# Kernel optimization log

Measured on AMD Instinct MI355X. Metric: run time of the kernel, lower is better.

The kernel has to match this reference:

```python
import jax, jax.numpy as jnp
import numpy as np

N = 100000      # total sampled nodes
NT = 20000      # target (destination) nodes
E = 2000000     # edges
IN = 128        # in_dim
OUT = 64        # out_channels (heads=1, concat)
NEG_SLOPE = 0.2 # GATConv default negative_slope


def setup_inputs() -> dict:
    key = jax.random.key(0)
    ks = jax.random.split(key, 6)
    x = jax.random.normal(ks[0], (N, IN), dtype=jnp.float32)
    edge_src = jax.random.randint(ks[1], (E,), 0, N)
    edge_dst = jax.random.randint(ks[2], (E,), 0, NT)
    # GATConv params: shared lin for src/dst (in_channels is int), att vectors, bias
    W = jax.random.normal(ks[3], (IN, OUT), dtype=jnp.float32) / np.sqrt(IN).astype(np.float32)
    att_src = jax.random.normal(ks[4], (OUT,), dtype=jnp.float32)
    att_dst = jax.random.normal(ks[5], (OUT,), dtype=jnp.float32)
    bias = jnp.zeros((OUT,), dtype=jnp.float32)
    return {"x": x, "edge_src": edge_src, "edge_dst": edge_dst,
            "W": W, "att_src": att_src, "att_dst": att_dst, "bias": bias,
            "num_target": NT}


def reference(x, edge_src, edge_dst, W, att_src, att_dst, bias, num_target):
    # Linear transform (lin_src == lin_dst in PyG GATConv when in_channels is int)
    x_proj = x @ W                      # [N, OUT]
    x_dst = x_proj[:num_target]         # [NT, OUT] target nodes are x[:num_target]
    # Per-node attention logits
    a_src = x_proj @ att_src            # [N]
    a_dst = x_dst @ att_dst             # [NT]
    # Edge logits + LeakyReLU
    e = jax.nn.leaky_relu(a_src[edge_src] + a_dst[edge_dst], NEG_SLOPE)  # [E]
    # Segment softmax over edges grouped by destination
    m = jax.ops.segment_max(e, edge_dst, num_segments=num_target)
    m = jnp.where(jnp.isneginf(m), jnp.float32(0.0), m)  # empty segments
    p = jnp.exp(e - m[edge_dst])
    denom = jax.ops.segment_sum(p, edge_dst, num_segments=num_target)
    alpha = p / (denom[edge_dst] + jnp.float32(1e-16))   # PyG softmax eps
    # Weighted scatter-aggregate of source features
    out = jax.ops.segment_sum(alpha[:, None] * x_proj[edge_src], edge_dst,
                              num_segments=num_target)   # [NT, OUT]
    return out + bias
```

## Files before the change

kernel.cpp:

```cpp
#include <hip/hip_runtime.h>

#define IN_DIM 128
#define OUT_DIM 64
#define NEG_SLOPE 0.2f

#define NBUCK 625
#define BCAP 4096
#define CHUNK 8192

typedef __attribute__((ext_vector_type(8))) short short8v;
typedef __attribute__((ext_vector_type(4))) float f32x4;

__device__ __forceinline__ unsigned pack_bf16(float a, float b) {
    unsigned ua = __float_as_uint(a), ub = __float_as_uint(b);
    ua += 0x7FFFu + ((ua >> 16) & 1u);
    ub += 0x7FFFu + ((ub >> 16) & 1u);
    return (ua >> 16) | (ub & 0xFFFF0000u);
}

__device__ __forceinline__ short8v mk8(unsigned a, unsigned b, unsigned c, unsigned d) {
    union { uint4 u; short8v s; } z;
    z.u = make_uint4(a, b, c, d);
    return z.s;
}

__device__ __forceinline__ int slice_of(unsigned src, float inv_sdiv) {
    int s = (int)((float)src * inv_sdiv);
    return s > 3 ? 3 : s;
}

__global__ __launch_bounds__(256) void prep_kernel(
    const float* __restrict__ W, unsigned* __restrict__ w_hi,
    unsigned* __restrict__ w_lo, int* __restrict__ bcursor)
{
    if (blockIdx.x == 4) {
        for (int i = threadIdx.x; i < NBUCK; i += 256) bcursor[i] = 0;
        return;
    }
    int g = blockIdx.x * 256 + threadIdx.x;
    int kb = g >> 6, col = g & 63;
    unsigned uh[4], ul[4];
#pragma unroll
    for (int i = 0; i < 4; ++i) {
        float a = W[(kb * 8 + 2 * i) * 64 + col];
        float b = W[(kb * 8 + 2 * i + 1) * 64 + col];
        unsigned h = pack_bf16(a, b);
        float la = a - __uint_as_float(h << 16);
        float lb = b - __uint_as_float(h & 0xFFFF0000u);
        uh[i] = h;
        ul[i] = pack_bf16(la, lb);
    }
    *(uint4*)(w_hi + g * 4) = make_uint4(uh[0], uh[1], uh[2], uh[3]);
    *(uint4*)(w_lo + g * 4) = make_uint4(ul[0], ul[1], ul[2], ul[3]);
}

__global__ __launch_bounds__(1024) void fused_kernel(
    const float* __restrict__ x,
    const unsigned* __restrict__ w_hi, const unsigned* __restrict__ w_lo,
    const float* __restrict__ att_src, const float* __restrict__ att_dst,
    const int* __restrict__ edge_src, const int* __restrict__ edge_dst,
    int* __restrict__ bcursor, unsigned* __restrict__ inter,
    unsigned* __restrict__ x_bf, float* __restrict__ a_src,
    float* __restrict__ a_dst, int N, int NT, int E, int nchunk)
{
    __shared__ __align__(16) union SMem {
        struct {
            unsigned stage[CHUNK];
            int hist[NBUCK];
            int loff[NBUCK];
            int gbase[NBUCK];
            int cur[NBUCK];
            int wsum[16];
        } p;
        float C[128 * 64];
    } U;

    const int t = threadIdx.x;

    if ((int)blockIdx.x < nchunk) {
        const int c0 = blockIdx.x * CHUNK;
        const int cnt = min(CHUNK, E - c0);

        for (int i = t; i < NBUCK; i += 1024) U.p.hist[i] = 0;
        __syncthreads();

        unsigned pk[8];
        int nmine = 0;
        const int i0 = 8 * t;
        if (i0 + 8 <= cnt) {
            int4 s0 = *(const int4*)(edge_src + c0 + i0);
            int4 s1 = *(const int4*)(edge_src + c0 + i0 + 4);
            int4 d0 = *(const int4*)(edge_dst + c0 + i0);
            int4 d1 = *(const int4*)(edge_dst + c0 + i0 + 4);
            pk[0] = ((unsigned)d0.x << 17) | (unsigned)s0.x;
            pk[1] = ((unsigned)d0.y << 17) | (unsigned)s0.y;
            pk[2] = ((unsigned)d0.z << 17) | (unsigned)s0.z;
            pk[3] = ((unsigned)d0.w << 17) | (unsigned)s0.w;
            pk[4] = ((unsigned)d1.x << 17) | (unsigned)s1.x;
            pk[5] = ((unsigned)d1.y << 17) | (unsigned)s1.y;
            pk[6] = ((unsigned)d1.z << 17) | (unsigned)s1.z;
            pk[7] = ((unsigned)d1.w << 17) | (unsigned)s1.w;
            nmine = 8;
        } else {
#pragma unroll
            for (int k = 0; k < 8; ++k) {
                int i = i0 + k;
                if (i < cnt) {
                    pk[k] = ((unsigned)edge_dst[c0 + i] << 17) | (unsigned)edge_src[c0 + i];
                    nmine = k + 1;
                }
            }
        }
#pragma unroll
        for (int k = 0; k < 8; ++k)
            if (k < nmine) atomicAdd(&U.p.hist[pk[k] >> 22], 1);
        __syncthreads();

        {
            const int lane = t & 63, w = t >> 6;
            int v = (t < NBUCK) ? U.p.hist[t] : 0;
            int scan = v;
#pragma unroll
            for (int off = 1; off < 64; off <<= 1) {
                int o = __shfl_up(scan, off);
                if (lane >= off) scan += o;
            }
            if (lane == 63) U.p.wsum[w] = scan;
            __syncthreads();
            int wpre = 0;
#pragma unroll
            for (int i = 0; i < 16; ++i)
                if (i < w) wpre += U.p.wsum[i];
            int excl = wpre + scan - v;
            if (t < NBUCK) {
                U.p.loff[t] = excl;
                U.p.cur[t]  = excl;
                if (v > 0) U.p.gbase[t] = t * BCAP + atomicAdd(&bcursor[t], v);
            }
        }
        __syncthreads();

#pragma unroll
        for (int k = 0; k < 8; ++k)
            if (k < nmine) {
                unsigned v = pk[k];
                int p = atomicAdd(&U.p.cur[v >> 22], 1);
                U.p.stage[p] = v;
            }
        __syncthreads();

        for (int i = t; i < cnt; i += 1024) {
            unsigned v = U.p.stage[i];
            int b = v >> 22;
            int pos = U.p.gbase[b] + (i - U.p.loff[b]);
            if (pos < (b + 1) * BCAP) inter[pos] = v;
        }
        return;
    }

    const int bid = blockIdx.x - nchunk;
    const int sub = t >> 8;
    const int t2  = t & 255;
    const int lane = t2 & 63;
    const int w    = t2 >> 6;
    const int r0   = bid * 512 + sub * 128;
    const int rsub = lane & 15;
    const int kg   = lane >> 4;

    const int r1 = min(r0 + 32 * w + rsub,      N - 1);
    const int r2 = min(r0 + 32 * w + 16 + rsub, N - 1);
    const float* xrow1 = x + (size_t)r1 * IN_DIM + kg * 8;
    const float* xrow2 = x + (size_t)r2 * IN_DIM + kg * 8;

    float4 xv[16];
#pragma unroll
    for (int j = 0; j < 8; ++j)
        xv[j] = *(const float4*)(xrow1 + (j >> 1) * 32 + (j & 1) * 4);
#pragma unroll
    for (int j = 0; j < 8; ++j)
        xv[8 + j] = *(const float4*)(xrow2 + (j >> 1) * 32 + (j & 1) * 4);
    __builtin_amdgcn_sched_barrier(0);

    short8v ah[2][4], al[2][4];
#pragma unroll
    for (int rf = 0; rf < 2; ++rf)
#pragma unroll
        for (int ks = 0; ks < 4; ++ks) {
            float4 v0 = xv[8 * rf + 2 * ks], v1 = xv[8 * rf + 2 * ks + 1];
            unsigned h0 = pack_bf16(v0.x, v0.y);
            unsigned h1 = pack_bf16(v0.z, v0.w);
            unsigned h2 = pack_bf16(v1.x, v1.y);
            unsigned h3 = pack_bf16(v1.z, v1.w);
            unsigned l0 = pack_bf16(v0.x - __uint_as_float(h0 << 16),
                                    v0.y - __uint_as_float(h0 & 0xFFFF0000u));
            unsigned l1 = pack_bf16(v0.z - __uint_as_float(h1 << 16),
                                    v0.w - __uint_as_float(h1 & 0xFFFF0000u));
            unsigned l2 = pack_bf16(v1.x - __uint_as_float(h2 << 16),
                                    v1.y - __uint_as_float(h2 & 0xFFFF0000u));
            unsigned l3 = pack_bf16(v1.z - __uint_as_float(h3 << 16),
                                    v1.w - __uint_as_float(h3 & 0xFFFF0000u));
            ah[rf][ks] = mk8(h0, h1, h2, h3);
            al[rf][ks] = mk8(l0, l1, l2, l3);
        }

    f32x4 acc[2][4];
#pragma unroll
    for (int rf = 0; rf < 2; ++rf)
#pragma unroll
        for (int cf = 0; cf < 4; ++cf) acc[rf][cf] = f32x4{0.f, 0.f, 0.f, 0.f};

#pragma unroll
    for (int ks = 0; ks < 4; ++ks) {
        const int kb = 4 * ks + kg;
        const unsigned* bhp = w_hi + (kb * 64 + rsub) * 4;
        const unsigned* blp = w_lo + (kb * 64 + rsub) * 4;
        short8v bh[4], bl[4];
#pragma unroll
        for (int cf = 0; cf < 4; ++cf) {
            bh[cf] = *(const short8v*)(bhp + cf * 64);
            bl[cf] = *(const short8v*)(blp + cf * 64);
        }
#pragma unroll
        for (int cf = 0; cf < 4; ++cf) {
#pragma unroll
            for (int rf = 0; rf < 2; ++rf) {
                acc[rf][cf] = __builtin_amdgcn_mfma_f32_16x16x32_bf16(ah[rf][ks], bh[cf], acc[rf][cf], 0, 0, 0);
                acc[rf][cf] = __builtin_amdgcn_mfma_f32_16x16x32_bf16(al[rf][ks], bh[cf], acc[rf][cf], 0, 0, 0);
                acc[rf][cf] = __builtin_amdgcn_mfma_f32_16x16x32_bf16(ah[rf][ks], bl[cf], acc[rf][cf], 0, 0, 0);
            }
        }
    }

    for (int ph = 0; ph < 4; ++ph) {
        if (sub == ph) {
#pragma unroll
            for (int rf = 0; rf < 2; ++rf)
#pragma unroll
                for (int cf = 0; cf < 4; ++cf)
#pragma unroll
                    for (int j = 0; j < 4; ++j) {
                        int row = 32 * w + 16 * rf + 4 * kg + j;
                        int col = 16 * cf + rsub;
                        U.C[row * 64 + ((col + 4 * row) & 63)] = acc[rf][cf][j];
                    }
        }
        __syncthreads();
        if (sub == ph) {
            const int row = t2 >> 1;
            const int h   = t2 & 1;
            const int rr  = r0 + row;
            float v[32];
#pragma unroll
            for (int j = 0; j < 8; ++j) {
                int s = (32 * h + 4 * j + 4 * row) & 63;
                float4 f = *(const float4*)(U.C + row * 64 + s);
                v[4 * j + 0] = f.x; v[4 * j + 1] = f.y;
                v[4 * j + 2] = f.z; v[4 * j + 3] = f.w;
            }
            if (rr < N) {
                unsigned pk[16];
#pragma unroll
                for (int m = 0; m < 16; ++m)
                    pk[m] = pack_bf16(v[2 * m], v[2 * m + 1]);
                unsigned* dst = x_bf + (size_t)rr * 32 + h * 16;
                *(uint4*)(dst + 0)  = make_uint4(pk[0], pk[1], pk[2], pk[3]);
                *(uint4*)(dst + 4)  = make_uint4(pk[4], pk[5], pk[6], pk[7]);
                *(uint4*)(dst + 8)  = make_uint4(pk[8], pk[9], pk[10], pk[11]);
                *(uint4*)(dst + 12) = make_uint4(pk[12], pk[13], pk[14], pk[15]);

                float ps = 0.f, pd = 0.f;
#pragma unroll
                for (int i = 0; i < 32; ++i) {
                    ps = fmaf(v[i], att_src[32 * h + i], ps);
                    pd = fmaf(v[i], att_dst[32 * h + i], pd);
                }
                ps += __shfl_xor(ps, 1);
                pd += __shfl_xor(pd, 1);
                if (h == 0) {
                    a_src[rr] = ps;
                    if (rr < NT) a_dst[rr] = pd;
                }
            }
        }
        __syncthreads();
    }
}

#define LRELU_EXP(a) __expf(((a) > 0.f ? (a) : NEG_SLOPE * (a)))

__global__ __launch_bounds__(512) void agg_kernel(
    const int* __restrict__ bcursor, const unsigned* __restrict__ inter,
    const float* __restrict__ a_src, const float* __restrict__ a_dst,
    const unsigned* __restrict__ x_bf, const float* __restrict__ bias,
    float* __restrict__ out, int NT, float inv_sdiv)
{
    __shared__ unsigned ssrc[BCAP];
    __shared__ int cnt[128], off_[128], cur[128];

    const int b = blockIdx.x;
    const int t = threadIdx.x;
    const int base = b * BCAP;
    const int n = min(bcursor[b], BCAP);

    for (int i = t; i < 128; i += 512) cnt[i] = 0;
    __syncthreads();

    unsigned ev[8];
    int kk[8];
#pragma unroll
    for (int k = 0; k < 8; ++k) {
        int i = t + 512 * k;
        ev[k] = 0xFFFFFFFFu;
        kk[k] = 0;
        if (i < n) {
            unsigned v = inter[base + i];
            ev[k] = v;
            kk[k] = (slice_of(v & 0x1FFFFu, inv_sdiv) << 5) | ((v >> 17) & 31);
            atomicAdd(&cnt[kk[k]], 1);
        }
    }
    __syncthreads();

    if (t == 0) {
        int r = 0;
#pragma unroll
        for (int j = 0; j < 128; ++j) { off_[j] = r; r += cnt[j]; }
    }
    __syncthreads();
    if (t < 128) cur[t] = off_[t];
    __syncthreads();

#pragma unroll
    for (int k = 0; k < 8; ++k)
        if (ev[k] != 0xFFFFFFFFu) {
            int p = atomicAdd(&cur[kk[k]], 1);
            ssrc[p] = ev[k] & 0x1FFFFu;
        }
    __syncthreads();

    const int lane = t & 63;
    const int w    = t >> 6;
    const int q    = lane >> 4;
    const int g    = (lane >> 3) & 1;
    const int sub  = lane & 7;

    const int ld  = 4 * w + q;
    const int tgt = b * 32 + ld;
    const float ad = (tgt < NT) ? a_dst[tgt] : 0.f;

    float dl = 0.f;
    float acc[8];
#pragma unroll
    for (int k = 0; k < 8; ++k) acc[k] = 0.f;

    for (int s = 0; s < 4; ++s) {
        const int key = (s << 5) | ld;
        const int lo = off_[key];
        const int nn = cnt[key];

        int ncmax = (nn + 15) >> 4;
        ncmax = max(ncmax, __shfl_xor(ncmax, 16));
        ncmax = max(ncmax, __shfl_xor(ncmax, 32));

        for (int c = 0; c < ncmax; ++c) {
            const int el = 16 * c + 8 * g + sub;
            const bool valid = el < nn;
            const int sA = valid ? (int)ssrc[lo + el] : 0;

            int s8[8];
#pragma unroll
            for (int j = 0; j < 8; ++j) s8[j] = __shfl(sA, 16 * q + 8 * g + j);

            uint4 v[8];
#pragma unroll
            for (int j = 0; j < 8; ++j)
                v[j] = *(const uint4*)(x_bf + (size_t)s8[j] * 32 + sub * 4);

            const float aA = a_src[sA];
            const float pA = valid ? LRELU_EXP(aA + ad) : 0.f;
            dl += pA;

            float p8[8];
#pragma unroll
            for (int j = 0; j < 8; ++j) p8[j] = __shfl(pA, 16 * q + 8 * g + j);

#pragma unroll
            for (int j = 0; j < 8; ++j) {
                const float p = p8[j];
                acc[0] = fmaf(p, __uint_as_float(v[j].x << 16), acc[0]);
                acc[1] = fmaf(p, __uint_as_float(v[j].x & 0xFFFF0000u), acc[1]);
                acc[2] = fmaf(p, __uint_as_float(v[j].y << 16), acc[2]);
                acc[3] = fmaf(p, __uint_as_float(v[j].y & 0xFFFF0000u), acc[3]);
                acc[4] = fmaf(p, __uint_as_float(v[j].z << 16), acc[4]);
                acc[5] = fmaf(p, __uint_as_float(v[j].z & 0xFFFF0000u), acc[5]);
                acc[6] = fmaf(p, __uint_as_float(v[j].w << 16), acc[6]);
                acc[7] = fmaf(p, __uint_as_float(v[j].w & 0xFFFF0000u), acc[7]);
            }
        }
    }

#pragma unroll
    for (int k = 0; k < 8; ++k) acc[k] += __shfl_xor(acc[k], 8);
    dl += __shfl_xor(dl, 1);
    dl += __shfl_xor(dl, 2);
    dl += __shfl_xor(dl, 4);
    dl += __shfl_xor(dl, 8);

    if (g == 0 && tgt < NT) {
        const float inv = 1.f / (dl + 1e-16f);
        float4 b0 = *(const float4*)(bias + sub * 8);
        float4 b1 = *(const float4*)(bias + sub * 8 + 4);
        float* o = out + (size_t)tgt * OUT_DIM + sub * 8;
        float4 o0, o1;
        o0.x = fmaf(acc[0], inv, b0.x); o0.y = fmaf(acc[1], inv, b0.y);
        o0.z = fmaf(acc[2], inv, b0.z); o0.w = fmaf(acc[3], inv, b0.w);
        o1.x = fmaf(acc[4], inv, b1.x); o1.y = fmaf(acc[5], inv, b1.y);
        o1.z = fmaf(acc[6], inv, b1.z); o1.w = fmaf(acc[7], inv, b1.w);
        *(float4*)(o)     = o0;
        *(float4*)(o + 4) = o1;
    }
}

extern "C" void kernel_launch(void* const* d_in, const int* in_sizes, int n_in,
                              void* d_out, int out_size, void* d_ws, size_t ws_size,
                              hipStream_t stream)
{
    const float* x        = (const float*)d_in[0];
    const int*   edge_src = (const int*)d_in[1];
    const int*   edge_dst = (const int*)d_in[2];
    const float* W        = (const float*)d_in[3];
    const float* att_src  = (const float*)d_in[4];
    const float* att_dst  = (const float*)d_in[5];
    const float* bias     = (const float*)d_in[6];

    const int N  = in_sizes[0] / IN_DIM;
    const int E  = in_sizes[1];
    const int NT = out_size / OUT_DIM;
    float* out = (float*)d_out;

    const int sdiv = (N + 3) / 4;
    const float inv_sdiv = 1.0f / (float)sdiv;

    auto align256 = [](size_t v) { return (v + 255) & ~(size_t)255; };
    char* w = (char*)d_ws;
    unsigned* x_bf   = (unsigned*)w;  w += align256((size_t)N * 32 * 4);
    float*    a_src  = (float*)w;     w += align256((size_t)N * 4);
    float*    a_dst  = (float*)w;     w += align256((size_t)NT * 4);
    int*      bcursor= (int*)w;       w += align256((size_t)NBUCK * 4);
    unsigned* w_hi   = (unsigned*)w;  w += align256((size_t)1024 * 16);
    unsigned* w_lo   = (unsigned*)w;  w += align256((size_t)1024 * 16);
    unsigned* inter  = (unsigned*)w;  w += align256((size_t)NBUCK * BCAP * 4);

    prep_kernel<<<5, 256, 0, stream>>>(W, w_hi, w_lo, bcursor);

    const int nchunk = (E + CHUNK - 1) / CHUNK;
    const int ngemm  = (N + 511) / 512;
    fused_kernel<<<nchunk + ngemm, 1024, 0, stream>>>(
        x, w_hi, w_lo, att_src, att_dst, edge_src, edge_dst,
        bcursor, inter, x_bf, a_src, a_dst, N, NT, E, nchunk);

    agg_kernel<<<NBUCK, 512, 0, stream>>>(
        bcursor, inter, a_src, a_dst, x_bf, bias, out, NT, inv_sdiv);
}
```

Measured before the change: 105.8 us.

## Shrink fused kernel blocks to 512 threads with smaller chunks and GEMM tiles

Halves the fused kernel's block size to 512 threads with launch bounds allowing two blocks per CU. Edge chunks shrink from 8192 to 4096 edges, and the histogram scan now handles two buckets per thread to still cover all 625 buckets. GEMM blocks now cover 128 rows, with each wave doing one 16-row MFMA tile instead of two, and each half-block has its own LDS output slab, so the serialized four-phase epilogue with repeated syncs goes away. The aim is more resident blocks and fewer barrier stalls, at the cost of twice as many blocks, more global atomics on bucket cursors, and less per-wave work to hide load latency.

```diff
diff --git a/kernel.cpp b/kernel.cpp
--- a/kernel.cpp
+++ b/kernel.cpp
@@ -6,7 +6,7 @@
 
 #define NBUCK 625
 #define BCAP 4096
-#define CHUNK 8192
+#define CHUNK2 4096
 
 typedef __attribute__((ext_vector_type(8))) short short8v;
 typedef __attribute__((ext_vector_type(4))) float f32x4;
@@ -54,7 +54,7 @@
     *(uint4*)(w_lo + g * 4) = make_uint4(ul[0], ul[1], ul[2], ul[3]);
 }
 
-__global__ __launch_bounds__(1024) void fused_kernel(
+__global__ __launch_bounds__(512, 2) void fused_kernel(
     const float* __restrict__ x,
     const unsigned* __restrict__ w_hi, const unsigned* __restrict__ w_lo,
     const float* __restrict__ att_src, const float* __restrict__ att_dst,
@@ -65,23 +65,23 @@
 {
     __shared__ __align__(16) union SMem {
         struct {
-            unsigned stage[CHUNK];
+            unsigned stage[CHUNK2];
             int hist[NBUCK];
             int loff[NBUCK];
             int gbase[NBUCK];
             int cur[NBUCK];
-            int wsum[16];
+            int wsum[8];
         } p;
-        float C[128 * 64];
+        float C[2 * 64 * 64];
     } U;
 
     const int t = threadIdx.x;
 
     if ((int)blockIdx.x < nchunk) {
-        const int c0 = blockIdx.x * CHUNK;
-        const int cnt = min(CHUNK, E - c0);
-
-        for (int i = t; i < NBUCK; i += 1024) U.p.hist[i] = 0;
+        const int c0 = blockIdx.x * CHUNK2;
+        const int cnt = min(CHUNK2, E - c0);
+
+        for (int i = t; i < NBUCK; i += 512) U.p.hist[i] = 0;
         __syncthreads();
 
         unsigned pk[8];
@@ -118,8 +118,17 @@
 
         {
             const int lane = t & 63, w = t >> 6;
-            int v = (t < NBUCK) ? U.p.hist[t] : 0;
-            int scan = v;
+            int tmp[2], vv[2];
+            int mysum = 0;
+#pragma unroll
+            for (int k = 0; k < 2; ++k) {
+                int idx = t * 2 + k;
+                int v = (idx < NBUCK) ? U.p.hist[idx] : 0;
+                vv[k] = v;
+                tmp[k] = mysum;
+                mysum += v;
+            }
+            int scan = mysum;
 #pragma unroll
             for (int off = 1; off < 64; off <<= 1) {
                 int o = __shfl_up(scan, off);
@@ -129,13 +138,19 @@
             __syncthreads();
             int wpre = 0;
 #pragma unroll
-            for (int i = 0; i < 16; ++i)
+            for (int i = 0; i < 8; ++i)
                 if (i < w) wpre += U.p.wsum[i];
-            int excl = wpre + scan - v;
-            if (t < NBUCK) {
-                U.p.loff[t] = excl;
-                U.p.cur[t]  = excl;
-                if (v > 0) U.p.gbase[t] = t * BCAP + atomicAdd(&bcursor[t], v);
+            int excl = wpre + scan - mysum;
+#pragma unroll
+            for (int k = 0; k < 2; ++k) {
+                int idx = t * 2 + k;
+                if (idx < NBUCK) {
+                    int e = excl + tmp[k];
+                    U.p.loff[idx] = e;
+                    U.p.cur[idx]  = e;
+                    if (vv[k] > 0)
+                        U.p.gbase[idx] = idx * BCAP + atomicAdd(&bcursor[idx], vv[k]);
+                }
             }
         }
         __syncthreads();
@@ -149,7 +164,7 @@
             }
         __syncthreads();
 
-        for (int i = t; i < cnt; i += 1024) {
+        for (int i = t; i < cnt; i += 512) {
             unsigned v = U.p.stage[i];
             int b = v >> 22;
             int pos = U.p.gbase[b] + (i - U.p.loff[b]);
@@ -158,56 +173,48 @@
         return;
     }
 
-    const int bid = blockIdx.x - nchunk;
-    const int sub = t >> 8;
-    const int t2  = t & 255;
+    const int bid  = blockIdx.x - nchunk;
+    const int sub  = t >> 8;
+    const int t2   = t & 255;
     const int lane = t2 & 63;
     const int w    = t2 >> 6;
-    const int r0   = bid * 512 + sub * 128;
+    const int r0   = bid * 128 + sub * 64;
     const int rsub = lane & 15;
     const int kg   = lane >> 4;
-
-    const int r1 = min(r0 + 32 * w + rsub,      N - 1);
-    const int r2 = min(r0 + 32 * w + 16 + rsub, N - 1);
+    float* Cs = U.C + sub * 64 * 64;
+
+    const int r1 = min(r0 + 16 * w + rsub, N - 1);
     const float* xrow1 = x + (size_t)r1 * IN_DIM + kg * 8;
-    const float* xrow2 = x + (size_t)r2 * IN_DIM + kg * 8;
-
-    float4 xv[16];
+
+    float4 xv[8];
 #pragma unroll
     for (int j = 0; j < 8; ++j)
         xv[j] = *(const float4*)(xrow1 + (j >> 1) * 32 + (j & 1) * 4);
-#pragma unroll
-    for (int j = 0; j < 8; ++j)
-        xv[8 + j] = *(const float4*)(xrow2 + (j >> 1) * 32 + (j & 1) * 4);
     __builtin_amdgcn_sched_barrier(0);
 
-    short8v ah[2][4], al[2][4];
-#pragma unroll
-    for (int rf = 0; rf < 2; ++rf)
-#pragma unroll
-        for (int ks = 0; ks < 4; ++ks) {
-            float4 v0 = xv[8 * rf + 2 * ks], v1 = xv[8 * rf + 2 * ks + 1];
-            unsigned h0 = pack_bf16(v0.x, v0.y);
-            unsigned h1 = pack_bf16(v0.z, v0.w);
-            unsigned h2 = pack_bf16(v1.x, v1.y);
-            unsigned h3 = pack_bf16(v1.z, v1.w);
-            unsigned l0 = pack_bf16(v0.x - __uint_as_float(h0 << 16),
-                                    v0.y - __uint_as_float(h0 & 0xFFFF0000u));
-            unsigned l1 = pack_bf16(v0.z - __uint_as_float(h1 << 16),
-                                    v0.w - __uint_as_float(h1 & 0xFFFF0000u));
-            unsigned l2 = pack_bf16(v1.x - __uint_as_float(h2 << 16),
-                                    v1.y - __uint_as_float(h2 & 0xFFFF0000u));
-            unsigned l3 = pack_bf16(v1.z - __uint_as_float(h3 << 16),
-                                    v1.w - __uint_as_float(h3 & 0xFFFF0000u));
-            ah[rf][ks] = mk8(h0, h1, h2, h3);
-            al[rf][ks] = mk8(l0, l1, l2, l3);
-        }
-
-    f32x4 acc[2][4];
-#pragma unroll
-    for (int rf = 0; rf < 2; ++rf)
-#pragma unroll
-        for (int cf = 0; cf < 4; ++cf) acc[rf][cf] = f32x4{0.f, 0.f, 0.f, 0.f};
+    short8v ah[4], al[4];
+#pragma unroll
+    for (int ks = 0; ks < 4; ++ks) {
+        float4 v0 = xv[2 * ks], v1 = xv[2 * ks + 1];
+        unsigned h0 = pack_bf16(v0.x, v0.y);
+        unsigned h1 = pack_bf16(v0.z, v0.w);
+        unsigned h2 = pack_bf16(v1.x, v1.y);
+        unsigned h3 = pack_bf16(v1.z, v1.w);
+        unsigned l0 = pack_bf16(v0.x - __uint_as_float(h0 << 16),
+                                v0.y - __uint_as_float(h0 & 0xFFFF0000u));
+        unsigned l1 = pack_bf16(v0.z - __uint_as_float(h1 << 16),
+                                v0.w - __uint_as_float(h1 & 0xFFFF0000u));
+        unsigned l2 = pack_bf16(v1.x - __uint_as_float(h2 << 16),
+                                v1.y - __uint_as_float(h2 & 0xFFFF0000u));
+        unsigned l3 = pack_bf16(v1.z - __uint_as_float(h3 << 16),
+                                v1.w - __uint_as_float(h3 & 0xFFFF0000u));
+        ah[ks] = mk8(h0, h1, h2, h3);
+        al[ks] = mk8(l0, l1, l2, l3);
+    }
+
+    f32x4 acc[4];
+#pragma unroll
+    for (int cf = 0; cf < 4; ++cf) acc[cf] = f32x4{0.f, 0.f, 0.f, 0.f};
 
 #pragma unroll
     for (int ks = 0; ks < 4; ++ks) {
@@ -222,67 +229,58 @@
         }
 #pragma unroll
         for (int cf = 0; cf < 4; ++cf) {
-#pragma unroll
-            for (int rf = 0; rf < 2; ++rf) {
-                acc[rf][cf] = __builtin_amdgcn_mfma_f32_16x16x32_bf16(ah[rf][ks], bh[cf], acc[rf][cf], 0, 0, 0);
-                acc[rf][cf] = __builtin_amdgcn_mfma_f32_16x16x32_bf16(al[rf][ks], bh[cf], acc[rf][cf], 0, 0, 0);
-                acc[rf][cf] = __builtin_amdgcn_mfma_f32_16x16x32_bf16(ah[rf][ks], bl[cf], acc[rf][cf], 0, 0, 0);
-            }
-        }
-    }
-
-    for (int ph = 0; ph < 4; ++ph) {
-        if (sub == ph) {
-#pragma unroll
-            for (int rf = 0; rf < 2; ++rf)
-#pragma unroll
-                for (int cf = 0; cf < 4; ++cf)
-#pragma unroll
-                    for (int j = 0; j < 4; ++j) {
-                        int row = 32 * w + 16 * rf + 4 * kg + j;
-                        int col = 16 * cf + rsub;
-                        U.C[row * 64 + ((col + 4 * row) & 63)] = acc[rf][cf][j];
-                    }
-        }
-        __syncthreads();
-        if (sub == ph) {
-            const int row = t2 >> 1;
-            const int h   = t2 & 1;
-            const int rr  = r0 + row;
-            float v[32];
-#pragma unroll
-            for (int j = 0; j < 8; ++j) {
-                int s = (32 * h + 4 * j + 4 * row) & 63;
-                float4 f = *(const float4*)(U.C + row * 64 + s);
-                v[4 * j + 0] = f.x; v[4 * j + 1] = f.y;
-                v[4 * j + 2] = f.z; v[4 * j + 3] = f.w;
-            }
-            if (rr < N) {
-                unsigned pk[16];
-#pragma unroll
-                for (int m = 0; m < 16; ++m)
-                    pk[m] = pack_bf16(v[2 * m], v[2 * m + 1]);
-                unsigned* dst = x_bf + (size_t)rr * 32 + h * 16;
-                *(uint4*)(dst + 0)  = make_uint4(pk[0], pk[1], pk[2], pk[3]);
-                *(uint4*)(dst + 4)  = make_uint4(pk[4], pk[5], pk[6], pk[7]);
-                *(uint4*)(dst + 8)  = make_uint4(pk[8], pk[9], pk[10], pk[11]);
-                *(uint4*)(dst + 12) = make_uint4(pk[12], pk[13], pk[14], pk[15]);
-
-                float ps = 0.f, pd = 0.f;
-#pragma unroll
-                for (int i = 0; i < 32; ++i) {
-                    ps = fmaf(v[i], att_src[32 * h + i], ps);
-                    pd = fmaf(v[i], att_dst[32 * h + i], pd);
-                }
-                ps += __shfl_xor(ps, 1);
-                pd += __shfl_xor(pd, 1);
-                if (h == 0) {
-                    a_src[rr] = ps;
-                    if (rr < NT) a_dst[rr] = pd;
-                }
-            }
-        }
-        __syncthreads();
+            acc[cf] = __builtin_amdgcn_mfma_f32_16x16x32_bf16(ah[ks], bh[cf], acc[cf], 0, 0, 0);
+            acc[cf] = __builtin_amdgcn_mfma_f32_16x16x32_bf16(al[ks], bh[cf], acc[cf], 0, 0, 0);
+            acc[cf] = __builtin_amdgcn_mfma_f32_16x16x32_bf16(ah[ks], bl[cf], acc[cf], 0, 0, 0);
+        }
+    }
+
+#pragma unroll
+    for (int cf = 0; cf < 4; ++cf)
+#pragma unroll
+        for (int j = 0; j < 4; ++j) {
+            int row = 16 * w + 4 * kg + j;
+            int col = 16 * cf + rsub;
+            Cs[row * 64 + ((col + 4 * row) & 63)] = acc[cf][j];
+        }
+    __syncthreads();
+
+    {
+        const int row = t2 >> 2;
+        const int h   = t2 & 3;
+        const int rr  = r0 + row;
+        float v[16];
+#pragma unroll
+        for (int j = 0; j < 4; ++j) {
+            int s = (16 * h + 4 * j + 4 * row) & 63;
+            float4 f = *(const float4*)(Cs + row * 64 + s);
+            v[4 * j + 0] = f.x; v[4 * j + 1] = f.y;
+            v[4 * j + 2] = f.z; v[4 * j + 3] = f.w;
+        }
+        if (rr < N) {
+            unsigned pk[8];
+#pragma unroll
+            for (int m = 0; m < 8; ++m)
+                pk[m] = pack_bf16(v[2 * m], v[2 * m + 1]);
+            unsigned* dst = x_bf + (size_t)rr * 32 + h * 8;
+            *(uint4*)(dst + 0) = make_uint4(pk[0], pk[1], pk[2], pk[3]);
+            *(uint4*)(dst + 4) = make_uint4(pk[4], pk[5], pk[6], pk[7]);
+
+            float ps = 0.f, pd = 0.f;
+#pragma unroll
+            for (int i = 0; i < 16; ++i) {
+                ps = fmaf(v[i], att_src[16 * h + i], ps);
+                pd = fmaf(v[i], att_dst[16 * h + i], pd);
+            }
+            ps += __shfl_xor(ps, 1);
+            ps += __shfl_xor(ps, 2);
+            pd += __shfl_xor(pd, 1);
+            pd += __shfl_xor(pd, 2);
+            if (h == 0) {
+                a_src[rr] = ps;
+                if (rr < NT) a_dst[rr] = pd;
+            }
+        }
     }
 }
 
@@ -453,9 +451,9 @@
 
     prep_kernel<<<5, 256, 0, stream>>>(W, w_hi, w_lo, bcursor);
 
-    const int nchunk = (E + CHUNK - 1) / CHUNK;
-    const int ngemm  = (N + 511) / 512;
-    fused_kernel<<<nchunk + ngemm, 1024, 0, stream>>>(
+    const int nchunk = (E + CHUNK2 - 1) / CHUNK2;
+    const int ngemm  = (N + 127) / 128;
+    fused_kernel<<<nchunk + ngemm, 512, 0, stream>>>(
         x, w_hi, w_lo, att_src, att_dst, edge_src, edge_dst,
         bcursor, inter, x_bf, a_src, a_dst, N, NT, E, nchunk);
 
```

Result: faster. 92.15 us (-12.9%).
